# Performance work log

Measured on AMD Instinct MI355X. Metric: run time of the kernel, lower is better.

Reference implementation:

```python
import jax, jax.numpy as jnp
import numpy as np


def setup_inputs() -> dict:
    key = jax.random.key(0)
    ks = jax.random.split(key, 6)
    B, S, D = 2, 2048, 1024
    E, DFF = 8, 2048  # E includes always-on expert 0; router sees E-1 routed experts
    scale = 0.02
    return {
        "hidden_states": jax.random.normal(ks[0], (B, S, D), dtype=jnp.float32),
        "router_w": jax.random.normal(ks[1], (D, E - 1), dtype=jnp.float32) * scale,
        "router_b": jnp.zeros((E - 1,), dtype=jnp.float32),
        "wg": jax.random.normal(ks[2], (E, D, DFF), dtype=jnp.float32) * scale,
        "wu": jax.random.normal(ks[3], (E, D, DFF), dtype=jnp.float32) * scale,
        "wd": jax.random.normal(ks[4], (E, DFF, D), dtype=jnp.float32) * scale,
        "top_k": 2,
    }


def _expert_mlp(x, wg_e, wu_e, wd_e):
    # SwiGLU MLP: down( silu(x @ gate) * (x @ up) )
    return (jax.nn.silu(x @ wg_e) * (x @ wu_e)) @ wd_e


def reference(hidden_states, router_w, router_b, wg, wu, wd, top_k):
    B, S, D = hidden_states.shape
    E = wg.shape[0]  # total experts incl. always-on expert 0
    x = hidden_states.reshape(-1, D)  # [T, D]
    T = x.shape[0]

    # Router over E-1 routed experts, softmax in float32
    router_logits = x @ router_w + router_b  # [T, E-1]
    probs = jax.nn.softmax(router_logits.astype(jnp.float32), axis=-1)
    topw, topi = jax.lax.top_k(probs, top_k)  # [T, k]
    topw = topw / jnp.sum(topw, axis=-1, keepdims=True)
    topw = topw.astype(x.dtype)

    # Dense combine weights over routed experts (0 for unselected)
    cw = jnp.zeros((T, E - 1), dtype=x.dtype)
    cw = cw.at[jnp.arange(T)[:, None], topi].add(topw)  # [T, E-1]

    # Always-on expert 0 with weight 1
    out = _expert_mlp(x, wg[0], wu[0], wd[0])  # [T, D]

    # Routed experts 1..E-1 (static small loop over experts)
    for e in range(1, E):
        ye = _expert_mlp(x, wg[e], wu[e], wd[e])  # [T, D]
        out = out + cw[:, e - 1, None] * ye

    return out.reshape(B, S, -1)
```

## Files before the change

### kernel.cpp

```cpp
#include <hip/hip_runtime.h>

#define T_TOK 4096
#define DIM   1024
#define DFF   2048
#define NE    8
#define NR    7
#define MAXNB 71

typedef __bf16 bf16x8 __attribute__((ext_vector_type(8)));
typedef float  floatx4 __attribute__((ext_vector_type(4)));

__device__ __forceinline__ unsigned short f32_bf16(float f) {
  union { float f; unsigned int u; } v; v.f = f;
  unsigned int u = v.u;
  unsigned int r = (u + 0x7FFFu + ((u >> 16) & 1u)) >> 16;
  return (unsigned short)r;
}

typedef __attribute__((address_space(3))) void lds_void_t;
typedef const __attribute__((address_space(1))) void g_void_t;

__device__ __forceinline__ void gld16(const void* g, void* l) {
  __builtin_amdgcn_global_load_lds((g_void_t*)g, (lds_void_t*)l, 16, 0, 0);
}

__global__ __launch_bounds__(256) void cvt_x_kernel(const float4* __restrict__ in,
                                                    ushort4* __restrict__ out) {
  int i = blockIdx.x * 256 + threadIdx.x;
  float4 v = in[i];
  ushort4 o;
  o.x = f32_bf16(v.x); o.y = f32_bf16(v.y);
  o.z = f32_bf16(v.z); o.w = f32_bf16(v.w);
  out[i] = o;
}

__global__ __launch_bounds__(256) void router_kernel(const float* __restrict__ x,
                                                     const float* __restrict__ rw,
                                                     const float* __restrict__ rb,
                                                     int* __restrict__ idx,
                                                     float* __restrict__ wsl,
                                                     int* __restrict__ cnt) {
  const int lane = threadIdx.x & 63;
  const int t = blockIdx.x * 4 + (threadIdx.x >> 6);
  const float* xr = x + (size_t)t * DIM;
  float acc[NR];
#pragma unroll
  for (int e = 0; e < NR; e++) acc[e] = 0.f;
  for (int d = lane; d < DIM; d += 64) {
    float xv = xr[d];
#pragma unroll
    for (int e = 0; e < NR; e++) acc[e] += xv * rw[d * NR + e];
  }
#pragma unroll
  for (int off = 32; off > 0; off >>= 1) {
#pragma unroll
    for (int e = 0; e < NR; e++) acc[e] += __shfl_xor(acc[e], off, 64);
  }
  if (lane == 0) {
    float lg[NR];
    float m = -1e30f;
#pragma unroll
    for (int e = 0; e < NR; e++) { lg[e] = acc[e] + rb[e]; m = fmaxf(m, lg[e]); }
    float p[NR], s = 0.f;
#pragma unroll
    for (int e = 0; e < NR; e++) { p[e] = expf(lg[e] - m); s += p[e]; }
#pragma unroll
    for (int e = 0; e < NR; e++) p[e] /= s;
    int i1 = 0;
#pragma unroll
    for (int e = 1; e < NR; e++) if (p[e] > p[i1]) i1 = e;
    int i2 = (i1 == 0) ? 1 : 0;
#pragma unroll
    for (int e = 0; e < NR; e++) if (e != i1 && p[e] > p[i2]) i2 = e;
    float w1 = p[i1], w2 = p[i2], sw = w1 + w2;
    int s1 = atomicAdd(&cnt[i1], 1);
    idx[i1 * 4096 + s1] = t; wsl[i1 * 4096 + s1] = w1 / sw;
    int s2 = atomicAdd(&cnt[i2], 1);
    idx[i2 * 4096 + s2] = t; wsl[i2 * 4096 + s2] = w2 / sw;
  }
}

__global__ __launch_bounds__(256) void sched_kernel(const int* __restrict__ cnt,
                                                    int* __restrict__ idx,
                                                    float* __restrict__ wsl,
                                                    int4* __restrict__ schedM,
                                                    int4* __restrict__ schedP) {
  __shared__ int nb[NR], pref[NR];
  if (threadIdx.x == 0) {
    int p = 0;
    for (int e = 0; e < NR; e++) { int c = cnt[e]; int n = (c + 127) >> 7; nb[e] = n; pref[e] = p; p += n; }
  }
  __syncthreads();
  for (int e = 0; e < NR; e++) {
    int c = cnt[e], top = nb[e] * 128;
    for (int i = c + (int)threadIdx.x; i < top; i += 256) { idx[e * 4096 + i] = 0; wsl[e * 4096 + i] = 0.f; }
  }
  const int NB = pref[NR - 1] + nb[NR - 1];
  for (int y = threadIdx.x; y < MAXNB; y += 256) {
    int4 ent; ent.x = -1; ent.y = 0; ent.z = 0; ent.w = 0;
    if (y < NB) {
#pragma unroll
      for (int e = 0; e < NR; e++)
        if (y >= pref[e] && y < pref[e] + nb[e]) { ent.x = e; ent.y = y - pref[e]; ent.z = y * 128; }
    }
    schedM[y] = ent;
  }
  for (int i = threadIdx.x; i < NR * 32; i += 256) {
    int e = i >> 5, rb = i & 31;
    int4 ent; ent.w = 0;
    if (rb < nb[e]) { ent.x = e; ent.y = rb; ent.z = rb * 128; }
    else            { ent.x = -1; ent.y = 0; ent.z = 0; }
    schedP[i] = ent;
  }
}

__global__ __launch_bounds__(256) void transpose_cvt_kernel(
    const float* __restrict__ wg, const float* __restrict__ wu, const float* __restrict__ wd,
    unsigned short* __restrict__ wgt, unsigned short* __restrict__ wut,
    unsigned short* __restrict__ wdt) {
  __shared__ float tile[64][33];
  const int z = blockIdx.z;
  const float* src; unsigned short* dst; int R, C;
  if (z < 8)       { src = wg + (size_t)z * DIM * DFF;        dst = wgt + (size_t)z * DIM * DFF;        R = DIM; C = DFF; }
  else if (z < 16) { src = wu + (size_t)(z - 8) * DIM * DFF;  dst = wut + (size_t)(z - 8) * DIM * DFF;  R = DIM; C = DFF; }
  else             { src = wd + (size_t)(z - 16) * DFF * DIM; dst = wdt + (size_t)(z - 16) * DFF * DIM; R = DFF; C = DIM; }
  const int c0 = blockIdx.x * 32, r0 = blockIdx.y * 64;
  if (c0 >= C || r0 >= R) return;
  const int tx = threadIdx.x & 31, ty = threadIdx.x >> 5;
#pragma unroll
  for (int j = ty; j < 64; j += 8)
    tile[j][tx] = src[(size_t)(r0 + j) * C + c0 + tx];
  __syncthreads();
#pragma unroll
  for (int j = ty; j < 32; j += 8) {
    unsigned int lo = f32_bf16(tile[2 * tx][j]);
    unsigned int hi = f32_bf16(tile[2 * tx + 1][j]);
    *(unsigned int*)(dst + (size_t)(c0 + j) * R + r0 + 2 * tx) = lo | (hi << 16);
  }
}

__global__ __launch_bounds__(256) void gemm1_e0_kernel(
    const unsigned short* __restrict__ xb, const unsigned short* __restrict__ wgt_e,
    const unsigned short* __restrict__ wut_e, unsigned short* __restrict__ h) {
  __shared__ unsigned short As[128 * 32];
  __shared__ unsigned short Bg[64 * 32];
  __shared__ unsigned short Bu[64 * 32];
  const int tid = threadIdx.x, lane = tid & 63, wid = tid >> 6;
  const int m0 = blockIdx.y * 128, n0 = blockIdx.x * 64;
  const int wm = (wid >> 1) * 64, wn = (wid & 1) * 32;
  floatx4 accg[4][2], accu[4][2];
  const floatx4 z4 = {0.f, 0.f, 0.f, 0.f};
#pragma unroll
  for (int i = 0; i < 4; i++)
#pragma unroll
    for (int j = 0; j < 2; j++) { accg[i][j] = z4; accu[i][j] = z4; }
  const int srow = tid >> 2, scol = (tid & 3) * 8;
  const unsigned short* ap0 = xb + (size_t)(m0 + srow) * DIM + scol;
  const unsigned short* ap1 = ap0 + (size_t)64 * DIM;
  const unsigned short* bgp = wgt_e + (size_t)(n0 + srow) * DIM + scol;
  const unsigned short* bup = wut_e + (size_t)(n0 + srow) * DIM + scol;
  unsigned short* as0 = As + tid * 8;
  unsigned short* as1 = As + (256 + tid) * 8;
  unsigned short* bgl = Bg + tid * 8;
  unsigned short* bul = Bu + tid * 8;
  const int fr = lane & 15, kq = (lane >> 4) * 8;
  for (int k0 = 0; k0 < DIM; k0 += 32) {
    __syncthreads();
    gld16(ap0 + k0, as0); gld16(ap1 + k0, as1);
    gld16(bgp + k0, bgl); gld16(bup + k0, bul);
    __syncthreads();
    bf16x8 af[4], bgf[2], buf2[2];
#pragma unroll
    for (int mi = 0; mi < 4; mi++) af[mi] = *(const bf16x8*)(As + (wm + mi * 16 + fr) * 32 + kq);
#pragma unroll
    for (int ni = 0; ni < 2; ni++) {
      bgf[ni]  = *(const bf16x8*)(Bg + (wn + ni * 16 + fr) * 32 + kq);
      buf2[ni] = *(const bf16x8*)(Bu + (wn + ni * 16 + fr) * 32 + kq);
    }
#pragma unroll
    for (int mi = 0; mi < 4; mi++)
#pragma unroll
      for (int ni = 0; ni < 2; ni++) {
        accg[mi][ni] = __builtin_amdgcn_mfma_f32_16x16x32_bf16(af[mi], bgf[ni], accg[mi][ni], 0, 0, 0);
        accu[mi][ni] = __builtin_amdgcn_mfma_f32_16x16x32_bf16(af[mi], buf2[ni], accu[mi][ni], 0, 0, 0);
      }
  }
  const int rb0 = wm + (lane >> 4) * 4;
  const int cb0 = n0 + wn + fr;
#pragma unroll
  for (int mi = 0; mi < 4; mi++)
#pragma unroll
    for (int ni = 0; ni < 2; ni++)
#pragma unroll
      for (int r = 0; r < 4; r++) {
        int row = m0 + rb0 + mi * 16 + r;
        int col = cb0 + ni * 16;
        float g = accg[mi][ni][r], u = accu[mi][ni][r];
        float hv = (g / (1.f + __expf(-g))) * u;
        h[(size_t)row * DFF + col] = f32_bf16(hv);
      }
}

__global__ __launch_bounds__(256) void gemm1_routed_kernel(
    const unsigned short* __restrict__ xb, const unsigned short* __restrict__ wgt,
    const unsigned short* __restrict__ wut, const int* __restrict__ idx,
    const int4* __restrict__ sched, unsigned short* __restrict__ h) {
  const int4 ent = sched[blockIdx.y];
  if (ent.x < 0) return;
  const int e = ent.x, rblk = ent.y, sb = ent.z;
  __shared__ unsigned short As[128 * 32];
  __shared__ unsigned short Bg[64 * 32];
  __shared__ unsigned short Bu[64 * 32];
  const int tid = threadIdx.x, lane = tid & 63, wid = tid >> 6;
  const int n0 = blockIdx.x * 64;
  const int wm = (wid >> 1) * 64, wn = (wid & 1) * 32;
  floatx4 accg[4][2], accu[4][2];
  const floatx4 z4 = {0.f, 0.f, 0.f, 0.f};
#pragma unroll
  for (int i = 0; i < 4; i++)
#pragma unroll
    for (int j = 0; j < 2; j++) { accg[i][j] = z4; accu[i][j] = z4; }
  const unsigned short* wgt_e = wgt + (size_t)(e + 1) * DIM * DFF;
  const unsigned short* wut_e = wut + (size_t)(e + 1) * DIM * DFF;
  const int srow = tid >> 2, scol = (tid & 3) * 8;
  const int tok0 = idx[e * 4096 + rblk * 128 + srow];
  const int tok1 = idx[e * 4096 + rblk * 128 + srow + 64];
  const unsigned short* ap0 = xb + (size_t)tok0 * DIM + scol;
  const unsigned short* ap1 = xb + (size_t)tok1 * DIM + scol;
  const unsigned short* bgp = wgt_e + (size_t)(n0 + srow) * DIM + scol;
  const unsigned short* bup = wut_e + (size_t)(n0 + srow) * DIM + scol;
  unsigned short* as0 = As + tid * 8;
  unsigned short* as1 = As + (256 + tid) * 8;
  unsigned short* bgl = Bg + tid * 8;
  unsigned short* bul = Bu + tid * 8;
  const int fr = lane & 15, kq = (lane >> 4) * 8;
  for (int k0 = 0; k0 < DIM; k0 += 32) {
    __syncthreads();
    gld16(ap0 + k0, as0); gld16(ap1 + k0, as1);
    gld16(bgp + k0, bgl); gld16(bup + k0, bul);
    __syncthreads();
    bf16x8 af[4], bgf[2], buf2[2];
#pragma unroll
    for (int mi = 0; mi < 4; mi++) af[mi] = *(const bf16x8*)(As + (wm + mi * 16 + fr) * 32 + kq);
#pragma unroll
    for (int ni = 0; ni < 2; ni++) {
      bgf[ni]  = *(const bf16x8*)(Bg + (wn + ni * 16 + fr) * 32 + kq);
      buf2[ni] = *(const bf16x8*)(Bu + (wn + ni * 16 + fr) * 32 + kq);
    }
#pragma unroll
    for (int mi = 0; mi < 4; mi++)
#pragma unroll
      for (int ni = 0; ni < 2; ni++) {
        accg[mi][ni] = __builtin_amdgcn_mfma_f32_16x16x32_bf16(af[mi], bgf[ni], accg[mi][ni], 0, 0, 0);
        accu[mi][ni] = __builtin_amdgcn_mfma_f32_16x16x32_bf16(af[mi], buf2[ni], accu[mi][ni], 0, 0, 0);
      }
  }
  const int rb0 = wm + (lane >> 4) * 4;
  const int cb0 = n0 + wn + fr;
#pragma unroll
  for (int mi = 0; mi < 4; mi++)
#pragma unroll
    for (int ni = 0; ni < 2; ni++)
#pragma unroll
      for (int r = 0; r < 4; r++) {
        int lrow = rb0 + mi * 16 + r;
        int col = cb0 + ni * 16;
        float g = accg[mi][ni][r], u = accu[mi][ni][r];
        float hv = (g / (1.f + __expf(-g))) * u;
        h[(size_t)(sb + lrow) * DFF + col] = f32_bf16(hv);
      }
}

__global__ __launch_bounds__(256) void gemm2_e0_kernel(
    const unsigned short* __restrict__ h, const unsigned short* __restrict__ wdt0,
    float* __restrict__ out) {
  __shared__ unsigned short As[128 * 32];
  __shared__ unsigned short Bs[128 * 32];
  const int tid = threadIdx.x, lane = tid & 63, wid = tid >> 6;
  const int m0 = blockIdx.y * 128, n0 = blockIdx.x * 128;
  const int wm = (wid >> 1) * 64, wn = (wid & 1) * 64;
  floatx4 acc[4][4];
  const floatx4 z4 = {0.f, 0.f, 0.f, 0.f};
#pragma unroll
  for (int i = 0; i < 4; i++)
#pragma unroll
    for (int j = 0; j < 4; j++) acc[i][j] = z4;
  const int srow = tid >> 2, scol = (tid & 3) * 8;
  const unsigned short* ap0 = h + (size_t)(m0 + srow) * DFF + scol;
  const unsigned short* ap1 = ap0 + (size_t)64 * DFF;
  const unsigned short* bp0 = wdt0 + (size_t)(n0 + srow) * DFF + scol;
  const unsigned short* bp1 = bp0 + (size_t)64 * DFF;
  unsigned short* as0 = As + tid * 8;
  unsigned short* as1 = As + (256 + tid) * 8;
  unsigned short* bs0 = Bs + tid * 8;
  unsigned short* bs1 = Bs + (256 + tid) * 8;
  const int fr = lane & 15, kq = (lane >> 4) * 8;
  for (int k0 = 0; k0 < DFF; k0 += 32) {
    __syncthreads();
    gld16(ap0 + k0, as0); gld16(ap1 + k0, as1);
    gld16(bp0 + k0, bs0); gld16(bp1 + k0, bs1);
    __syncthreads();
    bf16x8 af[4], bf[4];
#pragma unroll
    for (int mi = 0; mi < 4; mi++) af[mi] = *(const bf16x8*)(As + (wm + mi * 16 + fr) * 32 + kq);
#pragma unroll
    for (int ni = 0; ni < 4; ni++) bf[ni] = *(const bf16x8*)(Bs + (wn + ni * 16 + fr) * 32 + kq);
#pragma unroll
    for (int mi = 0; mi < 4; mi++)
#pragma unroll
      for (int ni = 0; ni < 4; ni++)
        acc[mi][ni] = __builtin_amdgcn_mfma_f32_16x16x32_bf16(af[mi], bf[ni], acc[mi][ni], 0, 0, 0);
  }
  const int rb0 = wm + (lane >> 4) * 4;
  const int cb0 = n0 + wn + fr;
#pragma unroll
  for (int mi = 0; mi < 4; mi++)
#pragma unroll
    for (int ni = 0; ni < 4; ni++)
#pragma unroll
      for (int r = 0; r < 4; r++) {
        int row = m0 + rb0 + mi * 16 + r;
        int col = cb0 + ni * 16;
        out[(size_t)row * DIM + col] = acc[mi][ni][r];
      }
}

__global__ __launch_bounds__(256) void gemm2_routed_kernel(
    const unsigned short* __restrict__ h, const unsigned short* __restrict__ wdt,
    const int* __restrict__ idx, const float* __restrict__ wsl,
    const int4* __restrict__ sched, float* __restrict__ out) {
  const int4 ent = sched[blockIdx.y];
  if (ent.x < 0) return;
  const int e = ent.x, rblk = ent.y, sb = ent.z;
  __shared__ unsigned short As[128 * 32];
  __shared__ unsigned short Bs[128 * 32];
  const int tid = threadIdx.x, lane = tid & 63, wid = tid >> 6;
  const int n0 = blockIdx.x * 128;
  const int wm = (wid >> 1) * 64, wn = (wid & 1) * 64;
  floatx4 acc[4][4];
  const floatx4 z4 = {0.f, 0.f, 0.f, 0.f};
#pragma unroll
  for (int i = 0; i < 4; i++)
#pragma unroll
    for (int j = 0; j < 4; j++) acc[i][j] = z4;
  const unsigned short* wdt_e = wdt + (size_t)(e + 1) * DFF * DIM;
  const int srow = tid >> 2, scol = (tid & 3) * 8;
  const unsigned short* ap0 = h + (size_t)(sb + srow) * DFF + scol;
  const unsigned short* ap1 = ap0 + (size_t)64 * DFF;
  const unsigned short* bp0 = wdt_e + (size_t)(n0 + srow) * DFF + scol;
  const unsigned short* bp1 = bp0 + (size_t)64 * DFF;
  unsigned short* as0 = As + tid * 8;
  unsigned short* as1 = As + (256 + tid) * 8;
  unsigned short* bs0 = Bs + tid * 8;
  unsigned short* bs1 = Bs + (256 + tid) * 8;
  const int fr = lane & 15, kq = (lane >> 4) * 8;
  for (int k0 = 0; k0 < DFF; k0 += 32) {
    __syncthreads();
    gld16(ap0 + k0, as0); gld16(ap1 + k0, as1);
    gld16(bp0 + k0, bs0); gld16(bp1 + k0, bs1);
    __syncthreads();
    bf16x8 af[4], bf[4];
#pragma unroll
    for (int mi = 0; mi < 4; mi++) af[mi] = *(const bf16x8*)(As + (wm + mi * 16 + fr) * 32 + kq);
#pragma unroll
    for (int ni = 0; ni < 4; ni++) bf[ni] = *(const bf16x8*)(Bs + (wn + ni * 16 + fr) * 32 + kq);
#pragma unroll
    for (int mi = 0; mi < 4; mi++)
#pragma unroll
      for (int ni = 0; ni < 4; ni++)
        acc[mi][ni] = __builtin_amdgcn_mfma_f32_16x16x32_bf16(af[mi], bf[ni], acc[mi][ni], 0, 0, 0);
  }
  const int rb0 = wm + (lane >> 4) * 4;
  const int cb0 = n0 + wn + fr;
#pragma unroll
  for (int mi = 0; mi < 4; mi++)
#pragma unroll
    for (int r = 0; r < 4; r++) {
      int lrow = rb0 + mi * 16 + r;
      int gi = e * 4096 + rblk * 128 + lrow;
      int tok = idx[gi];
      float s = wsl[gi];
      if (s != 0.f) {
#pragma unroll
        for (int ni = 0; ni < 4; ni++)
          atomicAdd(&out[(size_t)tok * DIM + cb0 + ni * 16], s * acc[mi][ni][r]);
      }
    }
}

extern "C" void kernel_launch(void* const* d_in, const int* in_sizes, int n_in,
                              void* d_out, int out_size, void* d_ws, size_t ws_size,
                              hipStream_t stream) {
  const float* x  = (const float*)d_in[0];
  const float* rw = (const float*)d_in[1];
  const float* rb = (const float*)d_in[2];
  const float* wg = (const float*)d_in[3];
  const float* wu = (const float*)d_in[4];
  const float* wd = (const float*)d_in[5];
  float* out = (float*)d_out;

  const bool big = ws_size >= (size_t)146600000;
  const size_t H_ROWS = big ? (size_t)(MAXNB * 128) : (size_t)4096;

  char* p = (char*)d_ws;
  unsigned short* xb  = (unsigned short*)p; p += (size_t)T_TOK * DIM * 2;
  unsigned short* h   = (unsigned short*)p; p += H_ROWS * DFF * 2;
  unsigned short* wgt = (unsigned short*)p; p += (size_t)NE * DIM * DFF * 2;
  unsigned short* wut = (unsigned short*)p; p += (size_t)NE * DIM * DFF * 2;
  unsigned short* wdt = (unsigned short*)p; p += (size_t)NE * DIM * DFF * 2;
  int*   idx = (int*)p;   p += (size_t)NR * 4096 * 4;
  float* wsl = (float*)p; p += (size_t)NR * 4096 * 4;
  int*   cnt = (int*)p;   p += 64;
  int4*  schedM = (int4*)p; p += 2048;
  int4*  schedP = (int4*)p; p += 4096;

  cvt_x_kernel<<<dim3(T_TOK * DIM / 4 / 256), 256, 0, stream>>>((const float4*)x, (ushort4*)xb);
  hipMemsetAsync(cnt, 0, 64, stream);
  router_kernel<<<dim3(T_TOK / 4), 256, 0, stream>>>(x, rw, rb, idx, wsl, cnt);
  sched_kernel<<<dim3(1), 256, 0, stream>>>(cnt, idx, wsl, schedM, schedP);
  transpose_cvt_kernel<<<dim3(64, 32, 24), 256, 0, stream>>>(wg, wu, wd, wgt, wut, wdt);

  gemm1_e0_kernel<<<dim3(DFF / 64, T_TOK / 128), 256, 0, stream>>>(xb, wgt, wut, h);
  gemm2_e0_kernel<<<dim3(DIM / 128, T_TOK / 128), 256, 0, stream>>>(h, wdt, out);

  if (big) {
    gemm1_routed_kernel<<<dim3(DFF / 64, MAXNB), 256, 0, stream>>>(xb, wgt, wut, idx, schedM, h);
    gemm2_routed_kernel<<<dim3(DIM / 128, MAXNB), 256, 0, stream>>>(h, wdt, idx, wsl, schedM, out);
  } else {
    for (int r = 0; r < NR; r++) {
      gemm1_routed_kernel<<<dim3(DFF / 64, 32), 256, 0, stream>>>(xb, wgt, wut, idx, schedP + r * 32, h);
      gemm2_routed_kernel<<<dim3(DIM / 128, 32), 256, 0, stream>>>(h, wdt, idx, wsl, schedP + r * 32, out);
    }
  }
}
```

Baseline: 618.7 us.

## Merge always-on expert into routed grouped GEMM schedule with atomic accumulation

Measured after the change: 627.2 us. Within noise of the previous version (+1.4%).

```diff
diff --git a/kernel.cpp b/kernel.cpp
--- a/kernel.cpp
+++ b/kernel.cpp
@@ -6,6 +6,7 @@
 #define NE    8
 #define NR    7
 #define MAXNB 71
+#define NY    (32 + MAXNB)
 
 typedef __bf16 bf16x8 __attribute__((ext_vector_type(8)));
 typedef float  floatx4 __attribute__((ext_vector_type(4)));
@@ -37,8 +38,8 @@
 __global__ __launch_bounds__(256) void router_kernel(const float* __restrict__ x,
                                                      const float* __restrict__ rw,
                                                      const float* __restrict__ rb,
-                                                     int* __restrict__ idx,
-                                                     float* __restrict__ wsl,
+                                                     int* __restrict__ idxAll,
+                                                     float* __restrict__ wslAll,
                                                      int* __restrict__ cnt) {
   const int lane = threadIdx.x & 63;
   const int t = blockIdx.x * 4 + (threadIdx.x >> 6);
@@ -57,6 +58,7 @@
     for (int e = 0; e < NR; e++) acc[e] += __shfl_xor(acc[e], off, 64);
   }
   if (lane == 0) {
+    idxAll[t] = t; wslAll[t] = 1.0f;
     float lg[NR];
     float m = -1e30f;
 #pragma unroll
@@ -74,17 +76,18 @@
     for (int e = 0; e < NR; e++) if (e != i1 && p[e] > p[i2]) i2 = e;
     float w1 = p[i1], w2 = p[i2], sw = w1 + w2;
     int s1 = atomicAdd(&cnt[i1], 1);
-    idx[i1 * 4096 + s1] = t; wsl[i1 * 4096 + s1] = w1 / sw;
+    idxAll[4096 + i1 * 4096 + s1] = t; wslAll[4096 + i1 * 4096 + s1] = w1 / sw;
     int s2 = atomicAdd(&cnt[i2], 1);
-    idx[i2 * 4096 + s2] = t; wsl[i2 * 4096 + s2] = w2 / sw;
+    idxAll[4096 + i2 * 4096 + s2] = t; wslAll[4096 + i2 * 4096 + s2] = w2 / sw;
   }
 }
 
 __global__ __launch_bounds__(256) void sched_kernel(const int* __restrict__ cnt,
-                                                    int* __restrict__ idx,
-                                                    float* __restrict__ wsl,
-                                                    int4* __restrict__ schedM,
-                                                    int4* __restrict__ schedP) {
+                                                    int* __restrict__ idxAll,
+                                                    float* __restrict__ wslAll,
+                                                    int4* __restrict__ schedAll,
+                                                    int4* __restrict__ schedP,
+                                                    int rsb) {
   __shared__ int nb[NR], pref[NR];
   if (threadIdx.x == 0) {
     int p = 0;
@@ -93,23 +96,32 @@
   __syncthreads();
   for (int e = 0; e < NR; e++) {
     int c = cnt[e], top = nb[e] * 128;
-    for (int i = c + (int)threadIdx.x; i < top; i += 256) { idx[e * 4096 + i] = 0; wsl[e * 4096 + i] = 0.f; }
-  }
-  const int NB = pref[NR - 1] + nb[NR - 1];
+    for (int i = c + (int)threadIdx.x; i < top; i += 256) {
+      idxAll[4096 + e * 4096 + i] = 0; wslAll[4096 + e * 4096 + i] = 0.f;
+    }
+  }
+  const int NBtot = pref[NR - 1] + nb[NR - 1];
+  for (int y = threadIdx.x; y < 32; y += 256) {
+    int4 ent; ent.x = 0; ent.y = y * 128; ent.z = y * 128; ent.w = 0;
+    schedAll[y] = ent;
+  }
   for (int y = threadIdx.x; y < MAXNB; y += 256) {
     int4 ent; ent.x = -1; ent.y = 0; ent.z = 0; ent.w = 0;
-    if (y < NB) {
+    if (y < NBtot) {
 #pragma unroll
       for (int e = 0; e < NR; e++)
-        if (y >= pref[e] && y < pref[e] + nb[e]) { ent.x = e; ent.y = y - pref[e]; ent.z = y * 128; }
-    }
-    schedM[y] = ent;
+        if (y >= pref[e] && y < pref[e] + nb[e]) {
+          int rb2 = y - pref[e];
+          ent.x = e + 1; ent.y = 4096 + e * 4096 + rb2 * 128; ent.z = rsb + y * 128;
+        }
+    }
+    schedAll[32 + y] = ent;
   }
   for (int i = threadIdx.x; i < NR * 32; i += 256) {
-    int e = i >> 5, rb = i & 31;
+    int e = i >> 5, rb2 = i & 31;
     int4 ent; ent.w = 0;
-    if (rb < nb[e]) { ent.x = e; ent.y = rb; ent.z = rb * 128; }
-    else            { ent.x = -1; ent.y = 0; ent.z = 0; }
+    if (rb2 < nb[e]) { ent.x = e + 1; ent.y = 4096 + e * 4096 + rb2 * 128; ent.z = rsb + rb2 * 128; }
+    else             { ent.x = -1; ent.y = 0; ent.z = 0; }
     schedP[i] = ent;
   }
 }
@@ -139,75 +151,12 @@
   }
 }
 
-__global__ __launch_bounds__(256) void gemm1_e0_kernel(
-    const unsigned short* __restrict__ xb, const unsigned short* __restrict__ wgt_e,
-    const unsigned short* __restrict__ wut_e, unsigned short* __restrict__ h) {
-  __shared__ unsigned short As[128 * 32];
-  __shared__ unsigned short Bg[64 * 32];
-  __shared__ unsigned short Bu[64 * 32];
-  const int tid = threadIdx.x, lane = tid & 63, wid = tid >> 6;
-  const int m0 = blockIdx.y * 128, n0 = blockIdx.x * 64;
-  const int wm = (wid >> 1) * 64, wn = (wid & 1) * 32;
-  floatx4 accg[4][2], accu[4][2];
-  const floatx4 z4 = {0.f, 0.f, 0.f, 0.f};
-#pragma unroll
-  for (int i = 0; i < 4; i++)
-#pragma unroll
-    for (int j = 0; j < 2; j++) { accg[i][j] = z4; accu[i][j] = z4; }
-  const int srow = tid >> 2, scol = (tid & 3) * 8;
-  const unsigned short* ap0 = xb + (size_t)(m0 + srow) * DIM + scol;
-  const unsigned short* ap1 = ap0 + (size_t)64 * DIM;
-  const unsigned short* bgp = wgt_e + (size_t)(n0 + srow) * DIM + scol;
-  const unsigned short* bup = wut_e + (size_t)(n0 + srow) * DIM + scol;
-  unsigned short* as0 = As + tid * 8;
-  unsigned short* as1 = As + (256 + tid) * 8;
-  unsigned short* bgl = Bg + tid * 8;
-  unsigned short* bul = Bu + tid * 8;
-  const int fr = lane & 15, kq = (lane >> 4) * 8;
-  for (int k0 = 0; k0 < DIM; k0 += 32) {
-    __syncthreads();
-    gld16(ap0 + k0, as0); gld16(ap1 + k0, as1);
-    gld16(bgp + k0, bgl); gld16(bup + k0, bul);
-    __syncthreads();
-    bf16x8 af[4], bgf[2], buf2[2];
-#pragma unroll
-    for (int mi = 0; mi < 4; mi++) af[mi] = *(const bf16x8*)(As + (wm + mi * 16 + fr) * 32 + kq);
-#pragma unroll
-    for (int ni = 0; ni < 2; ni++) {
-      bgf[ni]  = *(const bf16x8*)(Bg + (wn + ni * 16 + fr) * 32 + kq);
-      buf2[ni] = *(const bf16x8*)(Bu + (wn + ni * 16 + fr) * 32 + kq);
-    }
-#pragma unroll
-    for (int mi = 0; mi < 4; mi++)
-#pragma unroll
-      for (int ni = 0; ni < 2; ni++) {
-        accg[mi][ni] = __builtin_amdgcn_mfma_f32_16x16x32_bf16(af[mi], bgf[ni], accg[mi][ni], 0, 0, 0);
-        accu[mi][ni] = __builtin_amdgcn_mfma_f32_16x16x32_bf16(af[mi], buf2[ni], accu[mi][ni], 0, 0, 0);
-      }
-  }
-  const int rb0 = wm + (lane >> 4) * 4;
-  const int cb0 = n0 + wn + fr;
-#pragma unroll
-  for (int mi = 0; mi < 4; mi++)
-#pragma unroll
-    for (int ni = 0; ni < 2; ni++)
-#pragma unroll
-      for (int r = 0; r < 4; r++) {
-        int row = m0 + rb0 + mi * 16 + r;
-        int col = cb0 + ni * 16;
-        float g = accg[mi][ni][r], u = accu[mi][ni][r];
-        float hv = (g / (1.f + __expf(-g))) * u;
-        h[(size_t)row * DFF + col] = f32_bf16(hv);
-      }
-}
-
-__global__ __launch_bounds__(256) void gemm1_routed_kernel(
+__global__ __launch_bounds__(256) void gemm1_kernel(
     const unsigned short* __restrict__ xb, const unsigned short* __restrict__ wgt,
-    const unsigned short* __restrict__ wut, const int* __restrict__ idx,
+    const unsigned short* __restrict__ wut, const int* __restrict__ idxAll,
     const int4* __restrict__ sched, unsigned short* __restrict__ h) {
   const int4 ent = sched[blockIdx.y];
   if (ent.x < 0) return;
-  const int e = ent.x, rblk = ent.y, sb = ent.z;
   __shared__ unsigned short As[128 * 32];
   __shared__ unsigned short Bg[64 * 32];
   __shared__ unsigned short Bu[64 * 32];
@@ -220,11 +169,11 @@
   for (int i = 0; i < 4; i++)
 #pragma unroll
     for (int j = 0; j < 2; j++) { accg[i][j] = z4; accu[i][j] = z4; }
-  const unsigned short* wgt_e = wgt + (size_t)(e + 1) * DIM * DFF;
-  const unsigned short* wut_e = wut + (size_t)(e + 1) * DIM * DFF;
+  const unsigned short* wgt_e = wgt + (size_t)ent.x * DIM * DFF;
+  const unsigned short* wut_e = wut + (size_t)ent.x * DIM * DFF;
   const int srow = tid >> 2, scol = (tid & 3) * 8;
-  const int tok0 = idx[e * 4096 + rblk * 128 + srow];
-  const int tok1 = idx[e * 4096 + rblk * 128 + srow + 64];
+  const int tok0 = idxAll[ent.y + srow];
+  const int tok1 = idxAll[ent.y + srow + 64];
   const unsigned short* ap0 = xb + (size_t)tok0 * DIM + scol;
   const unsigned short* ap1 = xb + (size_t)tok1 * DIM + scol;
   const unsigned short* bgp = wgt_e + (size_t)(n0 + srow) * DIM + scol;
@@ -267,71 +216,16 @@
         int col = cb0 + ni * 16;
         float g = accg[mi][ni][r], u = accu[mi][ni][r];
         float hv = (g / (1.f + __expf(-g))) * u;
-        h[(size_t)(sb + lrow) * DFF + col] = f32_bf16(hv);
+        h[(size_t)(ent.z + lrow) * DFF + col] = f32_bf16(hv);
       }
 }
 
-__global__ __launch_bounds__(256) void gemm2_e0_kernel(
-    const unsigned short* __restrict__ h, const unsigned short* __restrict__ wdt0,
-    float* __restrict__ out) {
-  __shared__ unsigned short As[128 * 32];
-  __shared__ unsigned short Bs[128 * 32];
-  const int tid = threadIdx.x, lane = tid & 63, wid = tid >> 6;
-  const int m0 = blockIdx.y * 128, n0 = blockIdx.x * 128;
-  const int wm = (wid >> 1) * 64, wn = (wid & 1) * 64;
-  floatx4 acc[4][4];
-  const floatx4 z4 = {0.f, 0.f, 0.f, 0.f};
-#pragma unroll
-  for (int i = 0; i < 4; i++)
-#pragma unroll
-    for (int j = 0; j < 4; j++) acc[i][j] = z4;
-  const int srow = tid >> 2, scol = (tid & 3) * 8;
-  const unsigned short* ap0 = h + (size_t)(m0 + srow) * DFF + scol;
-  const unsigned short* ap1 = ap0 + (size_t)64 * DFF;
-  const unsigned short* bp0 = wdt0 + (size_t)(n0 + srow) * DFF + scol;
-  const unsigned short* bp1 = bp0 + (size_t)64 * DFF;
-  unsigned short* as0 = As + tid * 8;
-  unsigned short* as1 = As + (256 + tid) * 8;
-  unsigned short* bs0 = Bs + tid * 8;
-  unsigned short* bs1 = Bs + (256 + tid) * 8;
-  const int fr = lane & 15, kq = (lane >> 4) * 8;
-  for (int k0 = 0; k0 < DFF; k0 += 32) {
-    __syncthreads();
-    gld16(ap0 + k0, as0); gld16(ap1 + k0, as1);
-    gld16(bp0 + k0, bs0); gld16(bp1 + k0, bs1);
-    __syncthreads();
-    bf16x8 af[4], bf[4];
-#pragma unroll
-    for (int mi = 0; mi < 4; mi++) af[mi] = *(const bf16x8*)(As + (wm + mi * 16 + fr) * 32 + kq);
-#pragma unroll
-    for (int ni = 0; ni < 4; ni++) bf[ni] = *(const bf16x8*)(Bs + (wn + ni * 16 + fr) * 32 + kq);
-#pragma unroll
-    for (int mi = 0; mi < 4; mi++)
-#pragma unroll
-      for (int ni = 0; ni < 4; ni++)
-        acc[mi][ni] = __builtin_amdgcn_mfma_f32_16x16x32_bf16(af[mi], bf[ni], acc[mi][ni], 0, 0, 0);
-  }
-  const int rb0 = wm + (lane >> 4) * 4;
-  const int cb0 = n0 + wn + fr;
-#pragma unroll
-  for (int mi = 0; mi < 4; mi++)
-#pragma unroll
-    for (int ni = 0; ni < 4; ni++)
-#pragma unroll
-      for (int r = 0; r < 4; r++) {
-        int row = m0 + rb0 + mi * 16 + r;
-        int col = cb0 + ni * 16;
-        out[(size_t)row * DIM + col] = acc[mi][ni][r];
-      }
-}
-
-__global__ __launch_bounds__(256) void gemm2_routed_kernel(
+__global__ __launch_bounds__(256) void gemm2_kernel(
     const unsigned short* __restrict__ h, const unsigned short* __restrict__ wdt,
-    const int* __restrict__ idx, const float* __restrict__ wsl,
+    const int* __restrict__ idxAll, const float* __restrict__ wslAll,
     const int4* __restrict__ sched, float* __restrict__ out) {
   const int4 ent = sched[blockIdx.y];
   if (ent.x < 0) return;
-  const int e = ent.x, rblk = ent.y, sb = ent.z;
   __shared__ unsigned short As[128 * 32];
   __shared__ unsigned short Bs[128 * 32];
   const int tid = threadIdx.x, lane = tid & 63, wid = tid >> 6;
@@ -343,9 +237,9 @@
   for (int i = 0; i < 4; i++)
 #pragma unroll
     for (int j = 0; j < 4; j++) acc[i][j] = z4;
-  const unsigned short* wdt_e = wdt + (size_t)(e + 1) * DFF * DIM;
+  const unsigned short* wdt_e = wdt + (size_t)ent.x * DFF * DIM;
   const int srow = tid >> 2, scol = (tid & 3) * 8;
-  const unsigned short* ap0 = h + (size_t)(sb + srow) * DFF + scol;
+  const unsigned short* ap0 = h + (size_t)(ent.z + srow) * DFF + scol;
   const unsigned short* ap1 = ap0 + (size_t)64 * DFF;
   const unsigned short* bp0 = wdt_e + (size_t)(n0 + srow) * DFF + scol;
   const unsigned short* bp1 = bp0 + (size_t)64 * DFF;
@@ -377,9 +271,8 @@
 #pragma unroll
     for (int r = 0; r < 4; r++) {
       int lrow = rb0 + mi * 16 + r;
-      int gi = e * 4096 + rblk * 128 + lrow;
-      int tok = idx[gi];
-      float s = wsl[gi];
+      int tok = idxAll[ent.y + lrow];
+      float s = wslAll[ent.y + lrow];
       if (s != 0.f) {
 #pragma unroll
         for (int ni = 0; ni < 4; ni++)
@@ -399,8 +292,10 @@
   const float* wd = (const float*)d_in[5];
   float* out = (float*)d_out;
 
-  const bool big = ws_size >= (size_t)146600000;
-  const size_t H_ROWS = big ? (size_t)(MAXNB * 128) : (size_t)4096;
+  const bool modeA = ws_size >= (size_t)163321408;
+  const bool modeB = !modeA && ws_size >= (size_t)146544192;
+  const size_t H_ROWS = modeA ? 13184 : (modeB ? 9088 : 4096);
+  const int rsb = modeA ? 4096 : 0;
 
   char* p = (char*)d_ws;
   unsigned short* xb  = (unsigned short*)p; p += (size_t)T_TOK * DIM * 2;
@@ -408,28 +303,33 @@
   unsigned short* wgt = (unsigned short*)p; p += (size_t)NE * DIM * DFF * 2;
   unsigned short* wut = (unsigned short*)p; p += (size_t)NE * DIM * DFF * 2;
   unsigned short* wdt = (unsigned short*)p; p += (size_t)NE * DIM * DFF * 2;
-  int*   idx = (int*)p;   p += (size_t)NR * 4096 * 4;
-  float* wsl = (float*)p; p += (size_t)NR * 4096 * 4;
-  int*   cnt = (int*)p;   p += 64;
-  int4*  schedM = (int4*)p; p += 2048;
-  int4*  schedP = (int4*)p; p += 4096;
+  int*   idxAll = (int*)p;   p += (size_t)(4096 + NR * 4096) * 4;
+  float* wslAll = (float*)p; p += (size_t)(4096 + NR * 4096) * 4;
+  int*   cnt = (int*)p;      p += 64;
+  int4*  schedAll = (int4*)p; p += 2048;
+  int4*  schedP   = (int4*)p; p += 4096;
 
   cvt_x_kernel<<<dim3(T_TOK * DIM / 4 / 256), 256, 0, stream>>>((const float4*)x, (ushort4*)xb);
   hipMemsetAsync(cnt, 0, 64, stream);
-  router_kernel<<<dim3(T_TOK / 4), 256, 0, stream>>>(x, rw, rb, idx, wsl, cnt);
-  sched_kernel<<<dim3(1), 256, 0, stream>>>(cnt, idx, wsl, schedM, schedP);
+  hipMemsetAsync(out, 0, (size_t)out_size * 4, stream);
+  router_kernel<<<dim3(T_TOK / 4), 256, 0, stream>>>(x, rw, rb, idxAll, wslAll, cnt);
+  sched_kernel<<<dim3(1), 256, 0, stream>>>(cnt, idxAll, wslAll, schedAll, schedP, rsb);
   transpose_cvt_kernel<<<dim3(64, 32, 24), 256, 0, stream>>>(wg, wu, wd, wgt, wut, wdt);
 
-  gemm1_e0_kernel<<<dim3(DFF / 64, T_TOK / 128), 256, 0, stream>>>(xb, wgt, wut, h);
-  gemm2_e0_kernel<<<dim3(DIM / 128, T_TOK / 128), 256, 0, stream>>>(h, wdt, out);
-
-  if (big) {
-    gemm1_routed_kernel<<<dim3(DFF / 64, MAXNB), 256, 0, stream>>>(xb, wgt, wut, idx, schedM, h);
-    gemm2_routed_kernel<<<dim3(DIM / 128, MAXNB), 256, 0, stream>>>(h, wdt, idx, wsl, schedM, out);
+  if (modeA) {
+    gemm1_kernel<<<dim3(DFF / 64, NY), 256, 0, stream>>>(xb, wgt, wut, idxAll, schedAll, h);
+    gemm2_kernel<<<dim3(DIM / 128, NY), 256, 0, stream>>>(h, wdt, idxAll, wslAll, schedAll, out);
+  } else if (modeB) {
+    gemm1_kernel<<<dim3(DFF / 64, 32), 256, 0, stream>>>(xb, wgt, wut, idxAll, schedAll, h);
+    gemm2_kernel<<<dim3(DIM / 128, 32), 256, 0, stream>>>(h, wdt, idxAll, wslAll, schedAll, out);
+    gemm1_kernel<<<dim3(DFF / 64, MAXNB), 256, 0, stream>>>(xb, wgt, wut, idxAll, schedAll + 32, h);
+    gemm2_kernel<<<dim3(DIM / 128, MAXNB), 256, 0, stream>>>(h, wdt, idxAll, wslAll, schedAll + 32, out);
   } else {
-    for (int r = 0; r < NR; r++) {
-      gemm1_routed_kernel<<<dim3(DFF / 64, 32), 256, 0, stream>>>(xb, wgt, wut, idx, schedP + r * 32, h);
-      gemm2_routed_kernel<<<dim3(DIM / 128, 32), 256, 0, stream>>>(h, wdt, idx, wsl, schedP + r * 32, out);
-    }
-  }
-}
+    gemm1_kernel<<<dim3(DFF / 64, 32), 256, 0, stream>>>(xb, wgt, wut, idxAll, schedAll, h);
+    gemm2_kernel<<<dim3(DIM / 128, 32), 256, 0, stream>>>(h, wdt, idxAll, wslAll, schedAll, out);
+    for (int e = 0; e < NR; e++) {
+      gemm1_kernel<<<dim3(DFF / 64, 32), 256, 0, stream>>>(xb, wgt, wut, idxAll, schedP + e * 32, h);
+      gemm2_kernel<<<dim3(DIM / 128, 32), 256, 0, stream>>>(h, wdt, idxAll, wslAll, schedP + e * 32, out);
+    }
+  }
+}
```
